# Performance work log

Hardware: AMD Instinct MI355X
Metric: run time of the kernel (lower is better)

## Reference

```python
import jax, jax.numpy as jnp
import numpy as np

T, HID, NH, HD, ROT, NSLOTS, B, S = 4096, 2048, 16, 128, 32, 16384, 2, 2048


def setup_inputs() -> dict:
    key = jax.random.key(0)
    ks = jax.random.split(key, 6)
    hidden_states = jax.random.normal(ks[0], (T, HID), jnp.float32)
    # per-sequence positions (2 sequences of length S), NeoX rotary freqs
    pos = jnp.tile(jnp.arange(S, dtype=jnp.float32), B)  # [T]
    inv_freq = 1.0 / (10000.0 ** (jnp.arange(0, ROT, 2, dtype=jnp.float32) / ROT))  # [ROT//2]
    ang = pos[:, None] * inv_freq[None, :]  # [T, ROT//2]
    cos, sin = jnp.cos(ang), jnp.sin(ang)
    w_qkv = jax.random.normal(ks[1], (3 * HID, HID), jnp.float32) * 0.02
    b_qkv = jax.random.normal(ks[2], (3 * HID,), jnp.float32) * 0.02
    w_dense = jax.random.normal(ks[3], (HID, HID), jnp.float32) * 0.02
    b_dense = jax.random.normal(ks[4], (HID,), jnp.float32) * 0.02
    k_cache = jnp.zeros((NSLOTS, NH, HD), jnp.float32)
    v_cache = jnp.zeros((NSLOTS, NH, HD), jnp.float32)
    slots = jnp.arange(T, dtype=jnp.int32)
    return {"hidden_states": hidden_states, "cos": cos, "sin": sin,
            "w_qkv": w_qkv, "b_qkv": b_qkv, "w_dense": w_dense, "b_dense": b_dense,
            "k_cache": k_cache, "v_cache": v_cache, "slots": slots,
            "batch": B, "seq_len": S}


def reference(hidden_states, cos, sin, w_qkv, b_qkv, w_dense, b_dense,
              k_cache, v_cache, slots, batch, seq_len):
    t, hid = hidden_states.shape
    nh, hd = k_cache.shape[1], k_cache.shape[2]
    rot = 2 * cos.shape[-1]

    # fused QKV projection; weight pre-permuted so output order is [3, H, D]
    qkv = (hidden_states @ w_qkv.T + b_qkv).reshape(t, 3, nh, hd)
    q, k, v = qkv[:, 0], qkv[:, 1], qkv[:, 2]

    # partial rotary embedding (NeoX rotate-half on the first `rot` dims)
    c = cos[:, None, :]  # [T,1,rot//2]
    s = sin[:, None, :]

    def rope(x):
        xr, xp = x[..., :rot], x[..., rot:]
        h = rot // 2
        x1, x2 = xr[..., :h], xr[..., h:]
        return jnp.concatenate([x1 * c - x2 * s, x2 * c + x1 * s, xp], axis=-1)

    q, k = rope(q), rope(k)

    # KV-cache store: slot-indexed scatter
    k_cache_new = k_cache.at[slots].set(k)
    v_cache_new = v_cache.at[slots].set(v)

    # prefill flash attention == causal SDPA over equal-length sequences
    scale = hd ** -0.5
    qb = q.reshape(batch, seq_len, nh, hd)
    kb = k.reshape(batch, seq_len, nh, hd)
    vb = v.reshape(batch, seq_len, nh, hd)
    scores = jnp.einsum('bqhd,bkhd->bhqk', qb, kb) * scale
    causal = jnp.tril(jnp.ones((seq_len, seq_len), bool))
    scores = jnp.where(causal[None, None], scores, jnp.finfo(scores.dtype).min)
    probs = jax.nn.softmax(scores, axis=-1)
    attn = jnp.einsum('bhqk,bkhd->bqhd', probs, vb).reshape(t, nh * hd)

    out = attn @ w_dense.T + b_dense
    return out, k_cache_new, v_cache_new
```

## Files before the change

kernel.cpp:

```cpp
#include <hip/hip_runtime.h>
#include <stdint.h>

typedef unsigned short u16;
typedef short short8 __attribute__((ext_vector_type(8)));
typedef float f32x4 __attribute__((ext_vector_type(4)));
typedef u16 u16x4 __attribute__((ext_vector_type(4)));
typedef const __attribute__((address_space(1))) unsigned int g_u32;
typedef __attribute__((address_space(3))) unsigned int l_u32;

#define T_TOK 4096
#define HID 2048
#define NHEAD 16
#define HD 128
#define NSLOTS 16384
#define BATCH 2
#define SEQ 2048
#define NQKV 6144

__device__ __forceinline__ float bf2f(u16 u) {
    union { unsigned int i; float f; } v; v.i = ((unsigned int)u) << 16; return v.f;
}
__device__ __forceinline__ u16 f2bf(float f) {
    union { float f; unsigned int i; } v; v.f = f;
    unsigned int u = v.i;
    return (u16)((u + 0x7FFFu + ((u >> 16) & 1u)) >> 16);
}
__device__ __forceinline__ void gld_lds16(const u16* gsrc, u16* ldst) {
    __builtin_amdgcn_global_load_lds((g_u32*)gsrc, (l_u32*)ldst, 16, 0, 0);
}

__global__ __launch_bounds__(256)
void f32_to_bf16(const float* __restrict__ src, u16* __restrict__ dst) {
    const long i = ((long)blockIdx.x * 256 + threadIdx.x) * 4;
    const f32x4 v = *(const f32x4*)&src[i];
    u16x4 o;
    o[0] = f2bf(v[0]); o[1] = f2bf(v[1]); o[2] = f2bf(v[2]); o[3] = f2bf(v[3]);
    *(u16x4*)&dst[i] = o;
}

template <bool OUTF32>
__global__ __launch_bounds__(256)
void gemm_bt_bias(const u16* __restrict__ A, int lda,
                  const u16* __restrict__ B, int ldb,
                  const float* __restrict__ bias, void* __restrict__ Cv, int ldc,
                  int M, int N, int K) {
    __shared__ __align__(16) u16 As[128 * 32];
    __shared__ __align__(16) u16 Bs[128 * 32];
    const int tid  = threadIdx.x;
    const int lane = tid & 63;
    const int wave = tid >> 6;
    const int quad = lane >> 4;
    const int l16  = lane & 15;
    const int wm   = wave & 1, wn = wave >> 1;
    const int m0 = blockIdx.y * 128;
    const int n0 = blockIdx.x * 128;

    f32x4 acc[4][4];
#pragma unroll
    for (int i = 0; i < 4; i++)
#pragma unroll
        for (int j = 0; j < 4; j++) acc[i][j] = (f32x4){0.f, 0.f, 0.f, 0.f};

    const int c0 = tid, c1 = tid + 256;
    const long aoff0 = (long)(m0 + (c0 >> 2)) * lda + ((c0 & 3) * 8);
    const long aoff1 = (long)(m0 + (c1 >> 2)) * lda + ((c1 & 3) * 8);
    const long boff0 = (long)(n0 + (c0 >> 2)) * ldb + ((c0 & 3) * 8);
    const long boff1 = (long)(n0 + (c1 >> 2)) * ldb + ((c1 & 3) * 8);

    for (int k0 = 0; k0 < K; k0 += 32) {
        gld_lds16(A + aoff0 + k0, &As[c0 * 8]);
        gld_lds16(A + aoff1 + k0, &As[c1 * 8]);
        gld_lds16(B + boff0 + k0, &Bs[c0 * 8]);
        gld_lds16(B + boff1 + k0, &Bs[c1 * 8]);
        __syncthreads();
        short8 af[4], bf[4];
#pragma unroll
        for (int mi = 0; mi < 4; mi++)
            af[mi] = *(const short8*)&As[(wm * 64 + mi * 16 + l16) * 32 + quad * 8];
#pragma unroll
        for (int ni = 0; ni < 4; ni++)
            bf[ni] = *(const short8*)&Bs[(wn * 64 + ni * 16 + l16) * 32 + quad * 8];
#pragma unroll
        for (int mi = 0; mi < 4; mi++)
#pragma unroll
            for (int ni = 0; ni < 4; ni++)
                acc[mi][ni] = __builtin_amdgcn_mfma_f32_16x16x32_bf16(af[mi], bf[ni], acc[mi][ni], 0, 0, 0);
        __syncthreads();
    }

#pragma unroll
    for (int mi = 0; mi < 4; mi++)
#pragma unroll
        for (int ni = 0; ni < 4; ni++) {
            const int col = n0 + wn * 64 + ni * 16 + l16;
            const float bv = bias[col];
#pragma unroll
            for (int r = 0; r < 4; r++) {
                const int row = m0 + wm * 64 + mi * 16 + quad * 4 + r;
                const float val = acc[mi][ni][r] + bv;
                if (OUTF32) ((float*)Cv)[(long)row * ldc + col] = val;
                else        ((u16*)Cv)[(long)row * ldc + col]  = f2bf(val);
            }
        }
}

__global__ __launch_bounds__(256)
void rope_stash_kernel(u16* __restrict__ qkv, const float* __restrict__ cosb,
                       const float* __restrict__ sinb, u16* __restrict__ vstash) {
    const int g = blockIdx.x * 256 + threadIdx.x;
    const int t = g >> 4, h = g & 15;
    u16* q = qkv + (size_t)t * NQKV + h * HD;
    u16* k = q + HID;
    u16* v = q + 2 * HID;
    u16* vs = vstash + (size_t)t * HID + h * HD;

    float c[16], s[16];
#pragma unroll
    for (int i = 0; i < 16; i++) { c[i] = cosb[t * 16 + i]; s[i] = sinb[t * 16 + i]; }
    {
        float x1[16], x2[16];
#pragma unroll
        for (int i = 0; i < 16; i++) { x1[i] = bf2f(q[i]); x2[i] = bf2f(q[i + 16]); }
#pragma unroll
        for (int i = 0; i < 16; i++) {
            q[i]      = f2bf(x1[i] * c[i] - x2[i] * s[i]);
            q[i + 16] = f2bf(x2[i] * c[i] + x1[i] * s[i]);
        }
    }
    {
        float x1[16], x2[16];
#pragma unroll
        for (int i = 0; i < 16; i++) { x1[i] = bf2f(k[i]); x2[i] = bf2f(k[i + 16]); }
#pragma unroll
        for (int i = 0; i < 16; i++) {
            k[i]      = f2bf(x1[i] * c[i] - x2[i] * s[i]);
            k[i + 16] = f2bf(x2[i] * c[i] + x1[i] * s[i]);
        }
    }
#pragma unroll
    for (int i = 0; i < 128; i += 4) *(u16x4*)&vs[i] = *(const u16x4*)&v[i];
}

__global__ __launch_bounds__(256)
void v_transpose(const u16* __restrict__ qkv, u16* __restrict__ vt) {
    __shared__ u16 lds[32][33];
    const int s0 = blockIdx.x * 32;
    const int d0 = blockIdx.y * 32;
    const int bh = blockIdx.z;
    const int b = bh >> 4, h = bh & 15;
    const int t = threadIdx.x;
    const int r = t >> 3;
    const int cc = (t & 7) * 4;
    const u16* src = qkv + (long)(b * SEQ + s0 + r) * NQKV + 2 * HID + h * HD + d0 + cc;
    u16x4 val = *(const u16x4*)src;
    lds[r][cc + 0] = val[0]; lds[r][cc + 1] = val[1];
    lds[r][cc + 2] = val[2]; lds[r][cc + 3] = val[3];
    __syncthreads();
    u16x4 o;
    o[0] = lds[cc + 0][r]; o[1] = lds[cc + 1][r];
    o[2] = lds[cc + 2][r]; o[3] = lds[cc + 3][r];
    u16* dst = vt + (long)bh * HD * SEQ + (long)(d0 + r) * SEQ + s0 + cc;
    *(u16x4*)dst = o;
}

__global__ __launch_bounds__(256)
void flash_attn(u16* __restrict__ qkv, const u16* __restrict__ vt) {
    __shared__ __align__(16) u16 Ks[32 * 128];
    __shared__ __align__(16) u16 Vs[128 * 32];
    __shared__ __align__(16) u16 Ps[4][16 * 32];
    const int tid  = threadIdx.x;
    const int lane = tid & 63;
    const int wave = tid >> 6;
    const int quad = lane >> 4;
    const int l16  = lane & 15;
    const int q0 = blockIdx.x * 64;
    const int bh = blockIdx.y;
    const int b = bh >> 4, h = bh & 15;
    const int qt = q0 + wave * 16;

    const u16* Qbase = qkv + (long)(b * SEQ) * NQKV + h * HD;
    const u16* Kbase = Qbase + HID;
    const u16* Vtb   = vt + (long)bh * HD * SEQ;

    short8 aq[4];
#pragma unroll
    for (int dk = 0; dk < 4; dk++)
        aq[dk] = *(const short8*)&Qbase[(long)(qt + l16) * NQKV + dk * 32 + quad * 8];

    f32x4 oacc[8];
#pragma unroll
    for (int i = 0; i < 8; i++) oacc[i] = (f32x4){0.f, 0.f, 0.f, 0.f};
    float m_old[4], l_run[4];
#pragma unroll
    for (int r = 0; r < 4; r++) { m_old[r] = -1e30f; l_run[r] = 0.f; }

    const int ntiles = q0 / 32 + 2;
    const float scale = 0.08838834764831845f;

    for (int kt = 0; kt < ntiles; kt++) {
        const int k0 = kt * 32;
        {
            int c = tid;
            gld_lds16(&Kbase[(long)(k0 + (c >> 4)) * NQKV + (c & 15) * 8], &Ks[c * 8]);
            gld_lds16(&Vtb[(long)(c >> 2) * SEQ + k0 + (c & 3) * 8], &Vs[c * 8]);
            c = tid + 256;
            gld_lds16(&Kbase[(long)(k0 + (c >> 4)) * NQKV + (c & 15) * 8], &Ks[c * 8]);
            gld_lds16(&Vtb[(long)(c >> 2) * SEQ + k0 + (c & 3) * 8], &Vs[c * 8]);
        }
        __syncthreads();

        f32x4 sacc[2];
        sacc[0] = (f32x4){0.f, 0.f, 0.f, 0.f};
        sacc[1] = (f32x4){0.f, 0.f, 0.f, 0.f};
#pragma unroll
        for (int dk = 0; dk < 4; dk++) {
            short8 bk0 = *(const short8*)&Ks[(l16) * 128 + dk * 32 + quad * 8];
            short8 bk1 = *(const short8*)&Ks[(16 + l16) * 128 + dk * 32 + quad * 8];
            sacc[0] = __builtin_amdgcn_mfma_f32_16x16x32_bf16(aq[dk], bk0, sacc[0], 0, 0, 0);
            sacc[1] = __builtin_amdgcn_mfma_f32_16x16x32_bf16(aq[dk], bk1, sacc[1], 0, 0, 0);
        }

        float sv[2][4];
#pragma unroll
        for (int st = 0; st < 2; st++)
#pragma unroll
            for (int r = 0; r < 4; r++) {
                float x = sacc[st][r] * scale;
                const int kg = k0 + st * 16 + l16;
                const int qg = qt + quad * 4 + r;
                if (kg > qg) x = -1e30f;
                sv[st][r] = x;
            }

        float alpha[4];
#pragma unroll
        for (int r = 0; r < 4; r++) {
            float mv = fmaxf(sv[0][r], sv[1][r]);
#pragma unroll
            for (int sh = 1; sh < 16; sh <<= 1) mv = fmaxf(mv, __shfl_xor(mv, sh));
            const float mnew = fmaxf(m_old[r], mv);
            alpha[r] = __expf(m_old[r] - mnew);
            const float p0 = __expf(sv[0][r] - mnew);
            const float p1 = __expf(sv[1][r] - mnew);
            sv[0][r] = p0; sv[1][r] = p1;
            float ls = p0 + p1;
#pragma unroll
            for (int sh = 1; sh < 16; sh <<= 1) ls += __shfl_xor(ls, sh);
            l_run[r] = l_run[r] * alpha[r] + ls;
            m_old[r] = mnew;
        }

#pragma unroll
        for (int dt = 0; dt < 8; dt++)
#pragma unroll
            for (int r = 0; r < 4; r++) oacc[dt][r] *= alpha[r];

#pragma unroll
        for (int st = 0; st < 2; st++)
#pragma unroll
            for (int r = 0; r < 4; r++)
                Ps[wave][(quad * 4 + r) * 32 + st * 16 + l16] = f2bf(sv[st][r]);
        __syncthreads();
        const short8 ap = *(const short8*)&Ps[wave][l16 * 32 + quad * 8];
#pragma unroll
        for (int dt = 0; dt < 8; dt++) {
            short8 bv = *(const short8*)&Vs[(dt * 16 + l16) * 32 + quad * 8];
            oacc[dt] = __builtin_amdgcn_mfma_f32_16x16x32_bf16(ap, bv, oacc[dt], 0, 0, 0);
        }
        __syncthreads();
    }

    u16* outp = qkv + (long)(b * SEQ + qt) * NQKV + 2 * HID + h * HD;
#pragma unroll
    for (int r = 0; r < 4; r++) {
        const float inv = 1.0f / fmaxf(l_run[r], 1e-30f);
#pragma unroll
        for (int dt = 0; dt < 8; dt++) {
            const int row = quad * 4 + r;
            const int col = dt * 16 + l16;
            outp[(long)row * NQKV + col] = f2bf(oacc[dt][r] * inv);
        }
    }
}

__global__ __launch_bounds__(256)
void scatter_k(const u16* __restrict__ qkv, const int* __restrict__ slots,
               float* __restrict__ outk) {
    const int g = blockIdx.x * 256 + threadIdx.x;
    const int t = g >> 4, h = g & 15;
    const u16* k = qkv + (size_t)t * NQKV + HID + h * HD;
    float* dst = outk + (size_t)slots[t] * HID + h * HD;
#pragma unroll
    for (int i = 0; i < 128; i += 4) {
        const u16x4 a = *(const u16x4*)&k[i];
        f32x4 f; f[0] = bf2f(a[0]); f[1] = bf2f(a[1]); f[2] = bf2f(a[2]); f[3] = bf2f(a[3]);
        *(f32x4*)&dst[i] = f;
    }
}

__global__ __launch_bounds__(256)
void scatter_v(const u16* __restrict__ vstash, const int* __restrict__ slots,
               float* __restrict__ outv) {
    const int g = blockIdx.x * 256 + threadIdx.x;
    const int t = g >> 4, h = g & 15;
    const u16* v = vstash + (size_t)t * HID + h * HD;
    float* dst = outv + (size_t)slots[t] * HID + h * HD;
#pragma unroll
    for (int i = 0; i < 128; i += 4) {
        const u16x4 a = *(const u16x4*)&v[i];
        f32x4 f; f[0] = bf2f(a[0]); f[1] = bf2f(a[1]); f[2] = bf2f(a[2]); f[3] = bf2f(a[3]);
        *(f32x4*)&dst[i] = f;
    }
}

extern "C" void kernel_launch(void* const* d_in, const int* in_sizes, int n_in,
                              void* d_out, int out_size, void* d_ws, size_t ws_size,
                              hipStream_t stream) {
    (void)in_sizes; (void)n_in; (void)out_size; (void)ws_size;
    const float* hidden  = (const float*)d_in[0];
    const float* cosb    = (const float*)d_in[1];
    const float* sinb    = (const float*)d_in[2];
    const float* w_qkv   = (const float*)d_in[3];
    const float* b_qkv   = (const float*)d_in[4];
    const float* w_dense = (const float*)d_in[5];
    const float* b_dense = (const float*)d_in[6];
    const float* k_cache = (const float*)d_in[7];
    const float* v_cache = (const float*)d_in[8];
    const int*   slots   = (const int*)d_in[9];

    float* out0 = (float*)d_out;
    float* outk = out0 + (size_t)T_TOK * HID;
    float* outv = outk + (size_t)NSLOTS * NHEAD * HD;

    u16* hidden_bf = (u16*)outk;
    u16* wqkv_bf   = hidden_bf + (size_t)T_TOK * HID;
    u16* vt        = wqkv_bf + (size_t)NQKV * HID;
    u16* wd_bf     = vt + (size_t)BATCH * NHEAD * HD * SEQ;
    u16* qkv       = (u16*)outv;
    u16* vstash    = (u16*)d_ws;

    f32_to_bf16<<<(T_TOK * HID) / 1024, 256, 0, stream>>>(hidden, hidden_bf);
    f32_to_bf16<<<(NQKV * HID) / 1024, 256, 0, stream>>>(w_qkv, wqkv_bf);
    f32_to_bf16<<<(HID * HID) / 1024, 256, 0, stream>>>(w_dense, wd_bf);

    dim3 g1(NQKV / 128, T_TOK / 128);
    gemm_bt_bias<false><<<g1, 256, 0, stream>>>(hidden_bf, HID, wqkv_bf, HID,
                                                b_qkv, qkv, NQKV, T_TOK, NQKV, HID);

    rope_stash_kernel<<<(T_TOK * NHEAD) / 256, 256, 0, stream>>>(qkv, cosb, sinb, vstash);

    dim3 g2(SEQ / 32, HD / 32, BATCH * NHEAD);
    v_transpose<<<g2, 256, 0, stream>>>(qkv, vt);

    dim3 g3(SEQ / 64, BATCH * NHEAD);
    flash_attn<<<g3, 256, 0, stream>>>(qkv, vt);

    dim3 g4(HID / 128, T_TOK / 128);
    gemm_bt_bias<true><<<g4, 256, 0, stream>>>(qkv + 2 * HID, NQKV, wd_bf, HID,
                                               b_dense, out0, HID, T_TOK, HID, HID);

    const size_t cache_bytes = (size_t)NSLOTS * NHEAD * HD * sizeof(float);
    hipMemcpyAsync(outk, k_cache, cache_bytes, hipMemcpyDeviceToDevice, stream);
    scatter_k<<<(T_TOK * NHEAD) / 256, 256, 0, stream>>>(qkv, slots, outk);
    hipMemcpyAsync(outv, v_cache, cache_bytes, hipMemcpyDeviceToDevice, stream);
    scatter_v<<<(T_TOK * NHEAD) / 256, 256, 0, stream>>>(vstash, slots, outv);
}
```

Before: 1.086 ms.

## Swizzle LDS layouts, widen attention KV tile to 64, reverse query-block order

The GEMM stores A/B tiles in LDS with an XOR swizzle on the 16-byte chunk index to avoid bank conflicts on MFMA fragment reads. Flash attention now processes 64 keys per iteration instead of 32, halving the loop trips and barriers, and uses XOR-swizzled K, V and P layouts in LDS. Query blocks are launched in reverse order so the longest causal blocks start first, which should balance the tail. The larger tiles raise LDS use per block, which may lower occupancy. The P writes also drop the barrier between writing and reading the per-wave P tile.

Result: faster. 949.1 us (-12.6%).

```diff
diff --git a/kernel.cpp b/kernel.cpp
--- a/kernel.cpp
+++ b/kernel.cpp
@@ -61,25 +61,29 @@
 #pragma unroll
         for (int j = 0; j < 4; j++) acc[i][j] = (f32x4){0.f, 0.f, 0.f, 0.f};
 
-    const int c0 = tid, c1 = tid + 256;
-    const long aoff0 = (long)(m0 + (c0 >> 2)) * lda + ((c0 & 3) * 8);
-    const long aoff1 = (long)(m0 + (c1 >> 2)) * lda + ((c1 & 3) * 8);
-    const long boff0 = (long)(n0 + (c0 >> 2)) * ldb + ((c0 & 3) * 8);
-    const long boff1 = (long)(n0 + (c1 >> 2)) * ldb + ((c1 & 3) * 8);
+    const int s0 = tid, s1 = tid + 256;
+    const int r0 = s0 >> 2, r1 = s1 >> 2;
+    const int cs0 = (s0 & 3) ^ ((r0 >> 1) & 3);
+    const int cs1 = (s1 & 3) ^ ((r1 >> 1) & 3);
+    const long aoff0 = (long)(m0 + r0) * lda + cs0 * 8;
+    const long aoff1 = (long)(m0 + r1) * lda + cs1 * 8;
+    const long boff0 = (long)(n0 + r0) * ldb + cs0 * 8;
+    const long boff1 = (long)(n0 + r1) * ldb + cs1 * 8;
+    const int rcp = (quad ^ ((l16 >> 1) & 3)) * 8;
 
     for (int k0 = 0; k0 < K; k0 += 32) {
-        gld_lds16(A + aoff0 + k0, &As[c0 * 8]);
-        gld_lds16(A + aoff1 + k0, &As[c1 * 8]);
-        gld_lds16(B + boff0 + k0, &Bs[c0 * 8]);
-        gld_lds16(B + boff1 + k0, &Bs[c1 * 8]);
+        gld_lds16(A + aoff0 + k0, &As[s0 * 8]);
+        gld_lds16(A + aoff1 + k0, &As[s1 * 8]);
+        gld_lds16(B + boff0 + k0, &Bs[s0 * 8]);
+        gld_lds16(B + boff1 + k0, &Bs[s1 * 8]);
         __syncthreads();
         short8 af[4], bf[4];
 #pragma unroll
         for (int mi = 0; mi < 4; mi++)
-            af[mi] = *(const short8*)&As[(wm * 64 + mi * 16 + l16) * 32 + quad * 8];
+            af[mi] = *(const short8*)&As[(wm * 64 + mi * 16 + l16) * 32 + rcp];
 #pragma unroll
         for (int ni = 0; ni < 4; ni++)
-            bf[ni] = *(const short8*)&Bs[(wn * 64 + ni * 16 + l16) * 32 + quad * 8];
+            bf[ni] = *(const short8*)&Bs[(wn * 64 + ni * 16 + l16) * 32 + rcp];
 #pragma unroll
         for (int mi = 0; mi < 4; mi++)
 #pragma unroll
@@ -165,15 +169,15 @@
 
 __global__ __launch_bounds__(256)
 void flash_attn(u16* __restrict__ qkv, const u16* __restrict__ vt) {
-    __shared__ __align__(16) u16 Ks[32 * 128];
-    __shared__ __align__(16) u16 Vs[128 * 32];
-    __shared__ __align__(16) u16 Ps[4][16 * 32];
+    __shared__ __align__(16) u16 Ks[64 * 128];
+    __shared__ __align__(16) u16 Vs[128 * 64];
+    __shared__ __align__(16) u16 Ps[4][16 * 64];
     const int tid  = threadIdx.x;
     const int lane = tid & 63;
     const int wave = tid >> 6;
     const int quad = lane >> 4;
     const int l16  = lane & 15;
-    const int q0 = blockIdx.x * 64;
+    const int q0 = ((int)gridDim.x - 1 - (int)blockIdx.x) * 64;
     const int bh = blockIdx.y;
     const int b = bh >> 4, h = bh & 15;
     const int qt = q0 + wave * 16;
@@ -194,56 +198,66 @@
 #pragma unroll
     for (int r = 0; r < 4; r++) { m_old[r] = -1e30f; l_run[r] = 0.f; }
 
-    const int ntiles = q0 / 32 + 2;
+    int ksr[4], ksc[4], vsr[4], vsc[4];
+#pragma unroll
+    for (int i = 0; i < 4; i++) {
+        const int s = i * 256 + tid;
+        ksr[i] = s >> 4; ksc[i] = (s & 15) ^ (ksr[i] & 7);
+        vsr[i] = s >> 3; vsc[i] = (s & 7) ^ (vsr[i] & 7);
+    }
+
+    const int ntiles = q0 / 64 + 1;
     const float scale = 0.08838834764831845f;
+    const int swz = (l16 & 7);
 
     for (int kt = 0; kt < ntiles; kt++) {
-        const int k0 = kt * 32;
-        {
-            int c = tid;
-            gld_lds16(&Kbase[(long)(k0 + (c >> 4)) * NQKV + (c & 15) * 8], &Ks[c * 8]);
-            gld_lds16(&Vtb[(long)(c >> 2) * SEQ + k0 + (c & 3) * 8], &Vs[c * 8]);
-            c = tid + 256;
-            gld_lds16(&Kbase[(long)(k0 + (c >> 4)) * NQKV + (c & 15) * 8], &Ks[c * 8]);
-            gld_lds16(&Vtb[(long)(c >> 2) * SEQ + k0 + (c & 3) * 8], &Vs[c * 8]);
+        const int k0 = kt * 64;
+#pragma unroll
+        for (int i = 0; i < 4; i++) {
+            gld_lds16(&Kbase[(long)(k0 + ksr[i]) * NQKV + ksc[i] * 8], &Ks[(i * 256 + tid) * 8]);
+            gld_lds16(&Vtb[(long)vsr[i] * SEQ + k0 + vsc[i] * 8], &Vs[(i * 256 + tid) * 8]);
         }
         __syncthreads();
 
-        f32x4 sacc[2];
-        sacc[0] = (f32x4){0.f, 0.f, 0.f, 0.f};
-        sacc[1] = (f32x4){0.f, 0.f, 0.f, 0.f};
+        f32x4 sacc[4];
+#pragma unroll
+        for (int st = 0; st < 4; st++) sacc[st] = (f32x4){0.f, 0.f, 0.f, 0.f};
 #pragma unroll
         for (int dk = 0; dk < 4; dk++) {
-            short8 bk0 = *(const short8*)&Ks[(l16) * 128 + dk * 32 + quad * 8];
-            short8 bk1 = *(const short8*)&Ks[(16 + l16) * 128 + dk * 32 + quad * 8];
-            sacc[0] = __builtin_amdgcn_mfma_f32_16x16x32_bf16(aq[dk], bk0, sacc[0], 0, 0, 0);
-            sacc[1] = __builtin_amdgcn_mfma_f32_16x16x32_bf16(aq[dk], bk1, sacc[1], 0, 0, 0);
-        }
-
-        float sv[2][4];
-#pragma unroll
-        for (int st = 0; st < 2; st++)
+            const int cp = ((dk * 4 + quad) ^ swz) * 8;
+#pragma unroll
+            for (int st = 0; st < 4; st++) {
+                const short8 bk = *(const short8*)&Ks[(st * 16 + l16) * 128 + cp];
+                sacc[st] = __builtin_amdgcn_mfma_f32_16x16x32_bf16(aq[dk], bk, sacc[st], 0, 0, 0);
+            }
+        }
+
+        float sv[4][4];
+#pragma unroll
+        for (int st = 0; st < 4; st++) {
+            const int kg = k0 + st * 16 + l16;
 #pragma unroll
             for (int r = 0; r < 4; r++) {
                 float x = sacc[st][r] * scale;
-                const int kg = k0 + st * 16 + l16;
-                const int qg = qt + quad * 4 + r;
-                if (kg > qg) x = -1e30f;
+                if (kg > qt + quad * 4 + r) x = -1e30f;
                 sv[st][r] = x;
             }
+        }
 
         float alpha[4];
 #pragma unroll
         for (int r = 0; r < 4; r++) {
-            float mv = fmaxf(sv[0][r], sv[1][r]);
+            float mv = fmaxf(fmaxf(sv[0][r], sv[1][r]), fmaxf(sv[2][r], sv[3][r]));
 #pragma unroll
             for (int sh = 1; sh < 16; sh <<= 1) mv = fmaxf(mv, __shfl_xor(mv, sh));
             const float mnew = fmaxf(m_old[r], mv);
             alpha[r] = __expf(m_old[r] - mnew);
-            const float p0 = __expf(sv[0][r] - mnew);
-            const float p1 = __expf(sv[1][r] - mnew);
-            sv[0][r] = p0; sv[1][r] = p1;
-            float ls = p0 + p1;
+            float ls = 0.f;
+#pragma unroll
+            for (int st = 0; st < 4; st++) {
+                const float p = __expf(sv[st][r] - mnew);
+                sv[st][r] = p; ls += p;
+            }
 #pragma unroll
             for (int sh = 1; sh < 16; sh <<= 1) ls += __shfl_xor(ls, sh);
             l_run[r] = l_run[r] * alpha[r] + ls;
@@ -256,16 +270,25 @@
             for (int r = 0; r < 4; r++) oacc[dt][r] *= alpha[r];
 
 #pragma unroll
-        for (int st = 0; st < 2; st++)
-#pragma unroll
-            for (int r = 0; r < 4; r++)
-                Ps[wave][(quad * 4 + r) * 32 + st * 16 + l16] = f2bf(sv[st][r]);
-        __syncthreads();
-        const short8 ap = *(const short8*)&Ps[wave][l16 * 32 + quad * 8];
+        for (int st = 0; st < 4; st++) {
+            const int cbase = st * 2 + (l16 >> 3);
+#pragma unroll
+            for (int r = 0; r < 4; r++) {
+                const int row = quad * 4 + r;
+                Ps[wave][row * 64 + (cbase ^ (row & 7)) * 8 + (l16 & 7)] = f2bf(sv[st][r]);
+            }
+        }
+        short8 ap[2];
+#pragma unroll
+        for (int kk = 0; kk < 2; kk++)
+            ap[kk] = *(const short8*)&Ps[wave][l16 * 64 + ((kk * 4 + quad) ^ swz) * 8];
 #pragma unroll
         for (int dt = 0; dt < 8; dt++) {
-            short8 bv = *(const short8*)&Vs[(dt * 16 + l16) * 32 + quad * 8];
-            oacc[dt] = __builtin_amdgcn_mfma_f32_16x16x32_bf16(ap, bv, oacc[dt], 0, 0, 0);
+#pragma unroll
+            for (int kk = 0; kk < 2; kk++) {
+                const short8 bv = *(const short8*)&Vs[(dt * 16 + l16) * 64 + ((kk * 4 + quad) ^ swz) * 8];
+                oacc[dt] = __builtin_amdgcn_mfma_f32_16x16x32_bf16(ap[kk], bv, oacc[dt], 0, 0, 0);
+            }
         }
         __syncthreads();
     }
@@ -275,11 +298,8 @@
     for (int r = 0; r < 4; r++) {
         const float inv = 1.0f / fmaxf(l_run[r], 1e-30f);
 #pragma unroll
-        for (int dt = 0; dt < 8; dt++) {
-            const int row = quad * 4 + r;
-            const int col = dt * 16 + l16;
-            outp[(long)row * NQKV + col] = f2bf(oacc[dt][r] * inv);
-        }
+        for (int dt = 0; dt < 8; dt++)
+            outp[(long)(quad * 4 + r) * NQKV + dt * 16 + l16] = f2bf(oacc[dt][r] * inv);
     }
 }
 
```
